# Optimization experiments

Measured on AMD Instinct MI355X. Metric: run time of the kernel, lower is better.

The kernel has to match this reference:

```python
import jax, jax.numpy as jnp
import numpy as np

N, D, K = 500000, 64, 1024


def setup_inputs() -> dict:
    key = jax.random.key(0)
    kx, kc = jax.random.split(key)
    x = jax.random.normal(kx, (N, D), dtype=jnp.float32)
    centers = jax.random.normal(kc, (K, D), dtype=jnp.float32)
    return {"x": x, "centers": centers}


def reference(x, centers):
    # KMeans.predict: ids = argmin_k cdist(x, centers).
    # sqrt is monotone, so argmin over squared distances is identical, and the
    # This avoids the N x K x D expansion; the N x K score matrix is the
    # memory-bound hot path a fused kernel would stream over.
    m2 = jnp.sum(centers * centers, axis=-1)          # [K]
    scores = m2[None, :] - 2.0 * (x @ centers.T)      # [N, K]
    ids = jnp.argmin(scores, axis=-1)                 # [N]
    return ids
```

## Files before the change

kernel.cpp:

```cpp
#include <hip/hip_runtime.h>
#include <hip/hip_bf16.h>


#define N_PTS 500000
#define DIM   64
#define K_CENT 1024
#define MARGIN 1.5e-2f

typedef _Float16 half8   __attribute__((ext_vector_type(8)));
typedef float    floatx16 __attribute__((ext_vector_type(16)));

__global__ void kmeans_m2pre(const float* __restrict__ centers,
                             double* __restrict__ m2d)
{
    const int c = blockIdx.x * 256 + threadIdx.x;
    if (c >= K_CENT) return;
    const float4* crow = (const float4*)(centers + (size_t)c * DIM);
    double s = 0.0;
    #pragma unroll
    for (int kc = 0; kc < 16; ++kc) {
        float4 v = crow[kc];
        double a = v.x, b = v.y, cc = v.z, d = v.w;
        s += a * a + b * b + cc * cc + d * d;
    }
    m2d[c] = s;
}

__launch_bounds__(512, 4)
__global__ void kmeans_pass1(const float* __restrict__ x,
                             const float* __restrict__ centers,
                             const double* __restrict__ m2d,
                             int* __restrict__ out,
                             int* __restrict__ counter,
                             int* __restrict__ ulist,
                             int capacity)
{
    __shared__ __align__(16) _Float16 ldsC[512 * 72];
    __shared__ __align__(64) float negm2p[512];

    const int tid  = threadIdx.x;
    const int lane = tid & 63;
    const int wave = tid >> 6;
    const int col  = lane & 31;
    const int h    = lane >> 5;

    const int p  = blockIdx.x * 256 + wave * 32 + col;
    const int pc = p > N_PTS - 1 ? N_PTS - 1 : p;

    half8 bh[4];
    {
        const float* xr = x + (size_t)pc * DIM + h * 8;
        #pragma unroll
        for (int c = 0; c < 4; ++c) {
            float4 f0 = *(const float4*)(xr + c * 16);
            float4 f1 = *(const float4*)(xr + c * 16 + 4);
            float v[8] = {f0.x, f0.y, f0.z, f0.w, f1.x, f1.y, f1.z, f1.w};
            half8 hi;
            #pragma unroll
            for (int j = 0; j < 8; ++j) hi[j] = (_Float16)v[j];
            bh[c] = hi;
        }
    }

    float m1 = -3.0e38f, m2 = -3.0e38f;
    int   ctb = 0;

    for (int s = 0; s < 2; ++s) {
        __syncthreads();
        {
            const int ch = tid & 7;
            #pragma unroll
            for (int it = 0; it < 8; ++it) {
                const int c = (tid >> 3) + it * 64;
                const float* src = centers + (size_t)(s * 512 + c) * DIM + ch * 8;
                float4 f0 = *(const float4*)(src);
                float4 f1 = *(const float4*)(src + 4);
                float v[8] = {f0.x, f0.y, f0.z, f0.w, f1.x, f1.y, f1.z, f1.w};
                half8 hi;
                #pragma unroll
                for (int j = 0; j < 8; ++j) hi[j] = (_Float16)v[j];
                *(half8*)&ldsC[c * 72 + ch * 8] = hi;
            }
            {
                const int r = tid & 31, ctl = tid >> 5;
                const int hp = (r >> 2) & 1, reg = (r & 3) | ((r >> 3) << 2);
                negm2p[ctl * 32 + hp * 16 + reg] =
                    -0.5f * (float)m2d[s * 512 + tid];
            }
        }
        __syncthreads();

        for (int ctl = 0; ctl < 16; ++ctl) {
            const int ct = s * 16 + ctl;
            floatx16 acc = *(const floatx16*)&negm2p[ctl * 32 + h * 16];

            const _Float16* ap = &ldsC[(ctl * 32 + col) * 72 + h * 8];
            #pragma unroll
            for (int c = 0; c < 4; ++c) {
                half8 a = *(const half8*)(ap + c * 16);
                acc = __builtin_amdgcn_mfma_f32_32x32x16_f16(a, bh[c], acc, 0, 0, 0);
            }

            const float pre = m1;
            #pragma unroll
            for (int i = 0; i < 16; ++i) {
                unsigned u = (__float_as_uint(acc[i]) & 0xFFFFFFF0u) | (unsigned)i;
                float k = __uint_as_float(u);
                m2 = fmaxf(m2, fminf(m1, k));
                m1 = fmaxf(m1, k);
            }
            ctb = (m1 > pre) ? ct : ctb;
        }
    }

    {
        unsigned u = __float_as_uint(m1);
        int reg = (int)(u & 15u);
        int row = (reg & 3) + 8 * (reg >> 2) + 4 * h;
        int cid = ctb * 32 + row;

        float o1 = __shfl_xor(m1, 32);
        float o2 = __shfl_xor(m2, 32);
        int  ocid = __shfl_xor(cid, 32);
        float nm2 = fmaxf(fmaxf(m2, o2), fminf(m1, o1));
        bool take = o1 > m1;
        float nm1 = take ? o1 : m1;
        int  ncid = take ? ocid : cid;

        if (h == 0 && p < N_PTS) {
            out[p] = ncid;
            if (nm1 - nm2 < MARGIN) {
                int slot = atomicAdd(counter, 1);
                if (slot < capacity) ulist[slot] = p;
            }
        }
    }
}

__launch_bounds__(256)
__global__ void kmeans_pass2(const float* __restrict__ x,
                             const float* __restrict__ centers,
                             const double* __restrict__ m2d,
                             int* __restrict__ out,
                             const int* __restrict__ counter,
                             const int* __restrict__ ulist,
                             int capacity)
{
    int count = *counter;
    if (count > capacity) count = capacity;

    const int tid   = threadIdx.x;
    const int lane  = tid & 63;
    const int q     = lane & 15;
    const int rg    = lane >> 4;
    const int waveg = (blockIdx.x * 256 + tid) >> 6;
    const int nwave = (gridDim.x * 256) >> 6;

    for (int u = waveg; u < count; u += nwave) {
        const int p = ulist[u];
        float4 xv = *(const float4*)(x + (size_t)p * DIM + q * 4);
        const double x0 = xv.x, x1 = xv.y, x2 = xv.z, x3 = xv.w;

        double bv = 1.0e300; int bi = 0;
        #pragma unroll 4
        for (int g = 0; g < 256; ++g) {
            const int row = g * 4 + rg;
            float4 cv = *(const float4*)(centers + (size_t)row * DIM + q * 4);
            double dot = (double)cv.x * x0 + (double)cv.y * x1
                       + (double)cv.z * x2 + (double)cv.w * x3;
            #pragma unroll
            for (int m = 1; m <= 8; m <<= 1)
                dot += __shfl_xor(dot, m);
            double s = m2d[row] - 2.0 * dot;
            if (s < bv || (s == bv && row < bi)) { bv = s; bi = row; }
        }
        #pragma unroll
        for (int m = 16; m <= 32; m <<= 1) {
            double ov = __shfl_xor(bv, m);
            int    oi = __shfl_xor(bi, m);
            if (ov < bv || (ov == bv && oi < bi)) { bv = ov; bi = oi; }
        }
        if (lane == 0) out[p] = bi;
    }
}

extern "C" void kernel_launch(void* const* d_in, const int* in_sizes, int n_in,
                              void* d_out, int out_size, void* d_ws, size_t ws_size,
                              hipStream_t stream)
{
    const float* x       = (const float*)d_in[0];
    const float* centers = (const float*)d_in[1];
    int*    out     = (int*)d_out;
    int*    counter = (int*)d_ws;
    double* m2d     = (double*)((char*)d_ws + 1024);
    int*    ulist   = (int*)((char*)d_ws + 1024 + 8192);
    int capacity = (int)((ws_size > 9216 + 64 ? ws_size - 9216 : 0) / sizeof(int));
    if (capacity > N_PTS) capacity = N_PTS;

    hipMemsetAsync(d_ws, 0, 64, stream);
    kmeans_m2pre<<<4, 256, 0, stream>>>(centers, m2d);
    dim3 g1((N_PTS + 255) / 256);
    kmeans_pass1<<<g1, 512, 0, stream>>>(x, centers, m2d, out, counter, ulist, capacity);
    kmeans_pass2<<<3072, 256, 0, stream>>>(x, centers, m2d, out, counter, ulist, capacity);
}
```

Before: 362.1 us.

## Precompute fp16 centers once and stream MFMA A operands from global instead of LDS

The prep kernel now also writes an fp16 copy of the centers into workspace. pass1 drops its 72KB LDS center tile and its per-block fp32-to-fp16 conversion, and instead loads the A fragments for each 32-center tile straight from global memory, where they should stay cached in L2. The m2 bias for all 1024 centers is staged once, leaving one barrier instead of four. This cuts LDS use, which should raise occupancy and remove repeated conversion work, at the cost of more global or L1 traffic per wave and exposed load latency inside the MFMA loop.

```diff
diff --git a/kernel.cpp b/kernel.cpp
--- a/kernel.cpp
+++ b/kernel.cpp
@@ -11,32 +11,39 @@
 typedef float    floatx16 __attribute__((ext_vector_type(16)));
 
 __global__ void kmeans_m2pre(const float* __restrict__ centers,
-                             double* __restrict__ m2d)
+                             double* __restrict__ m2d,
+                             _Float16* __restrict__ cf16)
 {
     const int c = blockIdx.x * 256 + threadIdx.x;
     if (c >= K_CENT) return;
     const float4* crow = (const float4*)(centers + (size_t)c * DIM);
+    _Float16* frow = cf16 + (size_t)c * DIM;
     double s = 0.0;
     #pragma unroll
-    for (int kc = 0; kc < 16; ++kc) {
-        float4 v = crow[kc];
-        double a = v.x, b = v.y, cc = v.z, d = v.w;
-        s += a * a + b * b + cc * cc + d * d;
+    for (int g = 0; g < 8; ++g) {
+        float4 f0 = crow[2 * g], f1 = crow[2 * g + 1];
+        double a = f0.x, b = f0.y, cc = f0.z, d = f0.w;
+        double e = f1.x, f = f1.y, gg = f1.z, hh = f1.w;
+        s += a * a + b * b + cc * cc + d * d + e * e + f * f + gg * gg + hh * hh;
+        float v[8] = {f0.x, f0.y, f0.z, f0.w, f1.x, f1.y, f1.z, f1.w};
+        half8 hi;
+        #pragma unroll
+        for (int j = 0; j < 8; ++j) hi[j] = (_Float16)v[j];
+        *(half8*)(frow + g * 8) = hi;
     }
     m2d[c] = s;
 }
 
 __launch_bounds__(512, 4)
 __global__ void kmeans_pass1(const float* __restrict__ x,
-                             const float* __restrict__ centers,
+                             const _Float16* __restrict__ cf16,
                              const double* __restrict__ m2d,
                              int* __restrict__ out,
                              int* __restrict__ counter,
                              int* __restrict__ ulist,
                              int capacity)
 {
-    __shared__ __align__(16) _Float16 ldsC[512 * 72];
-    __shared__ __align__(64) float negm2p[512];
+    __shared__ __align__(64) float negm2p[K_CENT];
 
     const int tid  = threadIdx.x;
     const int lane = tid & 63;
@@ -62,55 +69,41 @@
         }
     }
 
+    #pragma unroll
+    for (int i = 0; i < 2; ++i) {
+        const int idx = tid + i * 512;
+        const int r = idx & 31, ct = idx >> 5;
+        const int hp = (r >> 2) & 1, reg = (r & 3) | ((r >> 3) << 2);
+        negm2p[ct * 32 + hp * 16 + reg] = -0.5f * (float)m2d[idx];
+    }
+    __syncthreads();
+
     float m1 = -3.0e38f, m2 = -3.0e38f;
     int   ctb = 0;
 
-    for (int s = 0; s < 2; ++s) {
-        __syncthreads();
-        {
-            const int ch = tid & 7;
-            #pragma unroll
-            for (int it = 0; it < 8; ++it) {
-                const int c = (tid >> 3) + it * 64;
-                const float* src = centers + (size_t)(s * 512 + c) * DIM + ch * 8;
-                float4 f0 = *(const float4*)(src);
-                float4 f1 = *(const float4*)(src + 4);
-                float v[8] = {f0.x, f0.y, f0.z, f0.w, f1.x, f1.y, f1.z, f1.w};
-                half8 hi;
-                #pragma unroll
-                for (int j = 0; j < 8; ++j) hi[j] = (_Float16)v[j];
-                *(half8*)&ldsC[c * 72 + ch * 8] = hi;
-            }
-            {
-                const int r = tid & 31, ctl = tid >> 5;
-                const int hp = (r >> 2) & 1, reg = (r & 3) | ((r >> 3) << 2);
-                negm2p[ctl * 32 + hp * 16 + reg] =
-                    -0.5f * (float)m2d[s * 512 + tid];
-            }
-        }
-        __syncthreads();
-
-        for (int ctl = 0; ctl < 16; ++ctl) {
-            const int ct = s * 16 + ctl;
-            floatx16 acc = *(const floatx16*)&negm2p[ctl * 32 + h * 16];
-
-            const _Float16* ap = &ldsC[(ctl * 32 + col) * 72 + h * 8];
-            #pragma unroll
-            for (int c = 0; c < 4; ++c) {
-                half8 a = *(const half8*)(ap + c * 16);
-                acc = __builtin_amdgcn_mfma_f32_32x32x16_f16(a, bh[c], acc, 0, 0, 0);
-            }
-
-            const float pre = m1;
-            #pragma unroll
-            for (int i = 0; i < 16; ++i) {
-                unsigned u = (__float_as_uint(acc[i]) & 0xFFFFFFF0u) | (unsigned)i;
-                float k = __uint_as_float(u);
-                m2 = fmaxf(m2, fminf(m1, k));
-                m1 = fmaxf(m1, k);
-            }
-            ctb = (m1 > pre) ? ct : ctb;
-        }
+    #pragma unroll 2
+    for (int ct = 0; ct < 32; ++ct) {
+        const _Float16* ap = cf16 + ((size_t)(ct * 32 + col)) * DIM + h * 8;
+        half8 a0 = *(const half8*)(ap);
+        half8 a1 = *(const half8*)(ap + 16);
+        half8 a2 = *(const half8*)(ap + 32);
+        half8 a3 = *(const half8*)(ap + 48);
+
+        floatx16 acc = *(const floatx16*)&negm2p[ct * 32 + h * 16];
+        acc = __builtin_amdgcn_mfma_f32_32x32x16_f16(a0, bh[0], acc, 0, 0, 0);
+        acc = __builtin_amdgcn_mfma_f32_32x32x16_f16(a1, bh[1], acc, 0, 0, 0);
+        acc = __builtin_amdgcn_mfma_f32_32x32x16_f16(a2, bh[2], acc, 0, 0, 0);
+        acc = __builtin_amdgcn_mfma_f32_32x32x16_f16(a3, bh[3], acc, 0, 0, 0);
+
+        const float pre = m1;
+        #pragma unroll
+        for (int i = 0; i < 16; ++i) {
+            unsigned u = (__float_as_uint(acc[i]) & 0xFFFFFFF0u) | (unsigned)i;
+            float k = __uint_as_float(u);
+            m2 = fmaxf(m2, fminf(m1, k));
+            m1 = fmaxf(m1, k);
+        }
+        ctb = (m1 > pre) ? ct : ctb;
     }
 
     {
@@ -193,13 +186,18 @@
     int*    out     = (int*)d_out;
     int*    counter = (int*)d_ws;
     double* m2d     = (double*)((char*)d_ws + 1024);
-    int*    ulist   = (int*)((char*)d_ws + 1024 + 8192);
-    int capacity = (int)((ws_size > 9216 + 64 ? ws_size - 9216 : 0) / sizeof(int));
+    int*    ulist   = (int*)((char*)d_ws + 9216);
+
+    const size_t CF16_BYTES = (size_t)K_CENT * DIM * sizeof(_Float16);
+    size_t cfoff = (ws_size > CF16_BYTES + 9216 + 64)
+                 ? ((ws_size - CF16_BYTES) & ~(size_t)255) : 9216;
+    _Float16* cf16 = (_Float16*)((char*)d_ws + cfoff);
+    int capacity = (int)((cfoff > 9216 ? cfoff - 9216 : 0) / sizeof(int));
     if (capacity > N_PTS) capacity = N_PTS;
 
     hipMemsetAsync(d_ws, 0, 64, stream);
-    kmeans_m2pre<<<4, 256, 0, stream>>>(centers, m2d);
+    kmeans_m2pre<<<4, 256, 0, stream>>>(centers, m2d, cf16);
     dim3 g1((N_PTS + 255) / 256);
-    kmeans_pass1<<<g1, 512, 0, stream>>>(x, centers, m2d, out, counter, ulist, capacity);
+    kmeans_pass1<<<g1, 512, 0, stream>>>(x, cf16, m2d, out, counter, ulist, capacity);
     kmeans_pass2<<<3072, 256, 0, stream>>>(x, centers, m2d, out, counter, ulist, capacity);
 }
```

Measured after the change: 524.8 us. 1.45x slower.
